# Optimization experiments

Hardware: AMD Instinct MI355X
Metric: run time of the kernel (lower is better)

Reference implementation:

```python
import jax, jax.numpy as jnp
import numpy as np

B, L, H, G, NH, DH, FF = 16, 512, 1024, 2, 16, 64, 4096
DM = H // G          # per-group d_model = 512
LG = L // G          # inner attention seq len = 256
EPS = 1e-6


def _ln(x, g, b):
    m = x.mean(-1, keepdims=True)
    v = ((x - m) ** 2).mean(-1, keepdims=True)
    return (x - m) * jax.lax.rsqrt(v + EPS) * g + b


def setup_inputs() -> dict:
    key = jax.random.key(0)
    ks = jax.random.split(key, 12)
    sd = 0.02
    n = lambda k, sh: jax.random.normal(k, sh, jnp.float32) * sd
    return {
        "y": jax.random.normal(ks[0], (B, L, H), jnp.float32),
        "y_mask": jax.random.randint(ks[1], (B, 1, 1, LG), 0, 2).astype(bool),
        # MHAtt projections (operate on per-group d_model = DM)
        "Wv": n(ks[2], (DM, DM)), "bv": jnp.zeros((DM,), jnp.float32),
        "Wk": n(ks[3], (DM, DM)), "bk": jnp.zeros((DM,), jnp.float32),
        "Wq": n(ks[4], (DM, DM)), "bq": jnp.zeros((DM,), jnp.float32),
        # merge projection (full hidden)
        "Wm": n(ks[5], (H, H)), "bm": jnp.zeros((H,), jnp.float32),
        # GFFN: linear1 H->FF, linear2 grouped FF/G -> H/G
        "W1": n(ks[6], (H, FF)), "b1": jnp.zeros((FF,), jnp.float32),
        "W2": n(ks[7], (FF // G, H // G)), "b2": jnp.zeros((H // G,), jnp.float32),
        # LayerNorms
        "g1": jnp.ones((H,), jnp.float32), "beta1": jnp.zeros((H,), jnp.float32),
        "g2": jnp.ones((H,), jnp.float32), "beta2": jnp.zeros((H,), jnp.float32),
    }


def reference(y, y_mask, Wv, bv, Wk, bk, Wq, bq, Wm, bm, W1, b1, W2, b2,
              g1, beta1, g2, beta2):
    b, l, d = y.shape
    # group reshuffle: split channels into G groups, stack along batch
    yg = jnp.concatenate(jnp.split(y, G, axis=-1), axis=0)        # (b*G, l, DM)
    mask = jnp.tile(y_mask, (G, 1, 1, 1))                          # (b*G, 1, 1, l/G)

    # projections; view uses h*dh = H so inner seq becomes l/G
    q = (yg @ Wq + bq).reshape(b * G, -1, NH, DH).transpose(0, 2, 1, 3)  # (bG, NH, l/G, DH)
    k = (yg @ Wk + bk).reshape(b * G, -1, NH, DH).transpose(0, 2, 1, 3)
    v = (yg @ Wv + bv).reshape(b * G, -1, NH, DH).transpose(0, 2, 1, 3)

    scores = jnp.einsum('bhqd,bhkd->bhqk', q, k) / np.sqrt(DH)
    scores = jnp.where(mask, jnp.float32(-1e9), scores)
    att = jax.nn.softmax(scores, axis=-1)                          # dropout = identity (eval)
    ctx = jnp.einsum('bhqk,bhkd->bhqd', att, v)                    # (bG, NH, l/G, DH)
    ctx = ctx.transpose(0, 2, 1, 3).reshape(b * G, -1, DM)         # (bG, l, DM)

    atted = jnp.concatenate(jnp.split(ctx, G, axis=0), axis=-1)    # (b, l, H)
    atted = atted @ Wm + bm
    y1 = _ln(y + atted, g1, beta1)

    # GFFN
    h1 = jax.nn.relu(y1 @ W1 + b1)                                  # (b, l, FF)
    h2 = jnp.einsum('blgf,fo->blgo', h1.reshape(b, l, G, FF // G), W2) + b2
    ff = h2.reshape(b, l, H)
    return _ln(y1 + ff, g2, beta2)
```

## Files before the change

### kernel.cpp

```cpp
#include <hip/hip_runtime.h>
#include <stdint.h>

typedef unsigned short u16;
using us8   = __attribute__((ext_vector_type(8))) unsigned short;
using us4   = __attribute__((ext_vector_type(4))) unsigned short;
using bf16x8 = __attribute__((ext_vector_type(8))) __bf16;
using f32x4 = __attribute__((ext_vector_type(4))) float;

#define DEV static __device__ __forceinline__

DEV float bf2f(u16 u) { union { uint32_t i; float f; } v; v.i = (uint32_t)u << 16; return v.f; }
DEV u16 f2bf(float f) {
    union { float f; uint32_t i; } v; v.f = f;
    uint32_t u = v.i;
    return (u16)((u + 0x7FFFu + ((u >> 16) & 1u)) >> 16);
}

DEV void async16(const u16* g, u16* ldsbase)
{
    __builtin_amdgcn_global_load_lds((const __attribute__((address_space(1))) void*)g,
                                     (__attribute__((address_space(3))) void*)ldsbase, 16, 0, 0);
}

struct DetectArgs { const void* p[18]; int nw[18]; };

__global__ __launch_bounds__(256) void k_detect_all(DetectArgs a, int* flags)
{
    const int b = blockIdx.x;
    const int t = threadIdx.x;
    __shared__ int cnt[4];
    if (t < 4) cnt[t] = 0;
    __syncthreads();
    if (b == 1) {
        const uint8_t* m = (const uint8_t*)a.p[1];
        int c0 = 0, c1 = 0, c2 = 0, c3 = 0;
        for (int i = t; i < 4096; i += 256) {
            uint8_t v = m[i];
            int mod = i & 3;
            if (v == 0x3F && mod == 1) c0++;
            if (v == 0x3F && mod == 3) c1++;
            if (v == 1 && mod != 0) c2++;
            if (v == 1 && mod == 0) c3++;
        }
        atomicAdd(&cnt[0], c0); atomicAdd(&cnt[1], c1); atomicAdd(&cnt[2], c2); atomicAdd(&cnt[3], c3);
        __syncthreads();
        if (t == 0) {
            int mf;
            if (cnt[0] > 0) mf = 2;
            else if (cnt[1] > 0) mf = 3;
            else if (cnt[2] > 0) mf = 0;
            else if (cnt[3] > 0) mf = 1;
            else mf = 0;
            flags[1] = mf;
        }
    } else {
        const u16* p = (const u16*)a.p[b];
        int nw = a.nw[b];
        int nze = 0, pe = 0, nzo = 0;
        for (int i = t; i < nw; i += 256) {
            u16 w = p[i];
            if (w == 0) continue;
            int e = (w >> 7) & 0xFF;
            bool pl = (e >= 90 && e <= 140);
            if ((i & 1) == 0) { nze++; if (pl) pe++; }
            else nzo++;
        }
        atomicAdd(&cnt[0], nze); atomicAdd(&cnt[1], pe); atomicAdd(&cnt[2], nzo);
        __syncthreads();
        if (t == 0) {
            int f;
            if (cnt[0] > 0)      f = (cnt[1] * 10 >= cnt[0] * 6) ? 2 : 3;
            else if (cnt[2] > 0) f = 3;
            else                 f = 2;
            flags[b] = f;
        }
    }
}

__global__ __launch_bounds__(256) void k_expand_mask(const void* mask, const int* flag, float* mb)
{
    int i = blockIdx.x * 256 + threadIdx.x;
    if (i >= 4096) return;
    int f = *flag;
    bool on;
    if (f == 0)      on = ((const uint8_t*)mask)[i]  != 0;
    else if (f == 1) on = ((const int*)mask)[i]      != 0;
    else if (f == 2) on = ((const u16*)mask)[i]      != 0;
    else             on = ((const uint32_t*)mask)[i] != 0;
    mb[i] = on ? -1e9f : 0.0f;
}

__global__ __launch_bounds__(256) void k_convert_bf(const void* src, u16* dst, int n, const int* flag)
{
    int i = blockIdx.x * 256 + threadIdx.x;
    if (i >= n) return;
    if (*flag == 2) dst[i] = ((const u16*)src)[i];
    else            dst[i] = f2bf(((const float*)src)[i]);
}

struct TransArgs { const void* src[6]; u16* dst[6]; int R[6]; int C[6]; int flagidx[6]; int tstart[7]; };

__global__ __launch_bounds__(256) void k_transpose_all(TransArgs a, const int* flags)
{
    const int tb = blockIdx.x;
    int s = 0;
    while (tb >= a.tstart[s + 1]) s++;
    const int lt = tb - a.tstart[s];
    const int R = a.R[s], C = a.C[s];
    const int tilesX = C >> 5;
    const int ti = lt / tilesX, tj = lt - ti * tilesX;
    const int r0 = ti * 32, c0 = tj * 32;
    const bool isbf = (flags[a.flagidx[s]] == 2);
    const int t = threadIdx.x;
    const int j = t & 31, i0 = t >> 5;
    __shared__ u16 tile[32][33];
#pragma unroll
    for (int p = 0; p < 4; p++) {
        int r = r0 + i0 + p * 8;
        size_t idx = (size_t)r * C + c0 + j;
        u16 v = isbf ? ((const u16*)a.src[s])[idx] : f2bf(((const float*)a.src[s])[idx]);
        tile[i0 + p * 8][j] = v;
    }
    __syncthreads();
    u16* dst = a.dst[s];
#pragma unroll
    for (int p = 0; p < 4; p++) {
        int c = i0 + p * 8;
        dst[(size_t)(c0 + c) * R + r0 + j] = tile[j][c];
    }
}

struct ConvArgs { const void* src[10]; int flagidx[10]; int off[10]; int n[10]; };

__global__ __launch_bounds__(256) void k_convert_params(ConvArgs a, const int* flags, float* par)
{
    int i = blockIdx.x * 256 + threadIdx.x;
    if (i >= 11264) return;
    int s = 0;
    while (s < 9 && i >= a.off[s] + a.n[s]) s++;
    int j = i - a.off[s];
    float v;
    if (flags[a.flagidx[s]] == 2) v = bf2f(((const u16*)a.src[s])[j]);
    else                          v = ((const float*)a.src[s])[j];
    par[i] = v;
}

template<int BM, int BN, int WR, int WC, int TM, int TN>
DEV void gemm_tile(const u16* __restrict__ A, int lda,
                   const u16* __restrict__ Bt, int ldb, int K,
                   u16* As, u16* Bs, f32x4 (&acc)[TM][TN])
{
    const int t = threadIdx.x;
    const int lane = t & 63;
    const int wave = t >> 6;
    const int wr = wave / WC;
    const int wc = wave % WC;
    const int m16 = lane & 15;
    const int quad = lane >> 4;
    const int lr8 = lane >> 3;
    const int lsw = (((lane & 7) ^ lr8) << 3);

#pragma unroll
    for (int i = 0; i < TM; i++)
#pragma unroll
        for (int j = 0; j < TN; j++) {
            acc[i][j][0] = 0.f; acc[i][j][1] = 0.f; acc[i][j][2] = 0.f; acc[i][j][3] = 0.f;
        }

    for (int kb = 0; kb < K; kb += 64) {
#pragma unroll
        for (int i = 0; i < BM / 32; i++) {
            int chunk = wave * (BM / 32) + i;
            int r = chunk * 8 + lr8;
            async16(A + (size_t)r * lda + kb + lsw, As + chunk * 512);
        }
#pragma unroll
        for (int i = 0; i < BN / 32; i++) {
            int chunk = wave * (BN / 32) + i;
            int r = chunk * 8 + lr8;
            async16(Bt + (size_t)r * ldb + kb + lsw, Bs + chunk * 512);
        }
        __syncthreads();
#pragma unroll
        for (int ks = 0; ks < 2; ks++) {
            bf16x8 af[TM], bfr[TN];
#pragma unroll
            for (int i = 0; i < TM; i++) {
                int row = wr * TM * 16 + i * 16 + m16;
                int jq = ks * 4 + quad;
                af[i] = *(const bf16x8*)(As + row * 64 + ((jq ^ (row & 7)) << 3));
            }
#pragma unroll
            for (int j = 0; j < TN; j++) {
                int row = wc * TN * 16 + j * 16 + m16;
                int jq = ks * 4 + quad;
                bfr[j] = *(const bf16x8*)(Bs + row * 64 + ((jq ^ (row & 7)) << 3));
            }
#pragma unroll
            for (int i = 0; i < TM; i++)
#pragma unroll
                for (int j = 0; j < TN; j++)
                    acc[i][j] = __builtin_amdgcn_mfma_f32_16x16x32_bf16(af[i], bfr[j], acc[i][j], 0, 0, 0);
        }
        __syncthreads();
    }
}

template<bool RELU>
__global__ __launch_bounds__(256) void k_gemm_std(const u16* __restrict__ A, int lda,
                                                  const u16* __restrict__ Bt, int ldb,
                                                  const float* __restrict__ bias,
                                                  u16* __restrict__ C, int ldc, int K)
{
    __shared__ __align__(16) u16 As[128 * 64];
    __shared__ __align__(16) u16 Bs[128 * 64];
    const u16* Ab = A + (size_t)blockIdx.y * 128 * lda;
    const u16* Bb = Bt + (size_t)blockIdx.x * 128 * ldb;
    f32x4 acc[4][4];
    gemm_tile<128, 128, 2, 2, 4, 4>(Ab, lda, Bb, ldb, K, As, Bs, acc);

    const int t = threadIdx.x, lane = t & 63, wave = t >> 6;
    const int wr = wave >> 1, wc = wave & 1, m16 = lane & 15, quad = lane >> 4;
    const size_t rowBase = (size_t)blockIdx.y * 128 + wr * 64;
    const int colBase = blockIdx.x * 128 + wc * 64;
#pragma unroll
    for (int tm = 0; tm < 4; tm++)
#pragma unroll
        for (int tn = 0; tn < 4; tn++) {
            int col = colBase + tn * 16 + m16;
            float bv = bias ? bias[col] : 0.f;
#pragma unroll
            for (int r = 0; r < 4; r++) {
                size_t row = rowBase + tm * 16 + quad * 4 + r;
                float v = acc[tm][tn][r] + bv;
                if (RELU) v = fmaxf(v, 0.f);
                C[row * (size_t)ldc + col] = f2bf(v);
            }
        }
}

__global__ __launch_bounds__(256) void k_gemm_qkv(const u16* __restrict__ y_c,
                                                  const u16* __restrict__ WqT,
                                                  const u16* __restrict__ WkT,
                                                  const u16* __restrict__ WvT,
                                                  const float* __restrict__ biases,
                                                  u16* __restrict__ qp, u16* __restrict__ kp, u16* __restrict__ vp)
{
    __shared__ __align__(16) u16 As[128 * 64];
    __shared__ __align__(16) u16 Bs[128 * 64];
    const int z = blockIdx.z;
    const int mat = z % 3, g = z / 3;
    const u16* Bt = (mat == 0) ? WqT : (mat == 1) ? WkT : WvT;
    u16* out = ((mat == 0) ? qp : (mat == 1) ? kp : vp) + (size_t)g * 4194304;
    const float* bias = biases + mat * 512;
    const u16* Ab = y_c + g * 512 + (size_t)blockIdx.y * 128 * 1024;
    const u16* Bb = Bt + (size_t)blockIdx.x * 128 * 512;
    f32x4 acc[4][4];
    gemm_tile<128, 128, 2, 2, 4, 4>(Ab, 1024, Bb, 512, 512, As, Bs, acc);

    const int t = threadIdx.x, lane = t & 63, wave = t >> 6;
    const int wr = wave >> 1, wc = wave & 1, m16 = lane & 15, quad = lane >> 4;
    const size_t rowBase = (size_t)blockIdx.y * 128 + wr * 64;
    const int colBase = blockIdx.x * 128 + wc * 64;
#pragma unroll
    for (int tm = 0; tm < 4; tm++)
#pragma unroll
        for (int tn = 0; tn < 4; tn++) {
            int col = colBase + tn * 16 + m16;
            float bv = bias[col];
#pragma unroll
            for (int r = 0; r < 4; r++) {
                size_t row = rowBase + tm * 16 + quad * 4 + r;
                out[row * 512 + col] = f2bf(acc[tm][tn][r] + bv);
            }
        }
}

__global__ __launch_bounds__(256) void k_attn_scores(const u16* __restrict__ qproj,
                                                     const u16* __restrict__ kproj,
                                                     const float* __restrict__ maskb,
                                                     u16* __restrict__ P)
{
    __shared__ __align__(16) u16 As[64 * 64];
    __shared__ __align__(16) u16 Bs[256 * 64];
    __shared__ float smax[64][5];
    __shared__ float ssum[64][5];
    const int rt = blockIdx.x;
    const int z = blockIdx.y;
    const int bg = z >> 4, h = z & 15, hbit = h >> 3, hlow = h & 7;
    const int b = bg & 15;
    const size_t base = (size_t)bg * 262144 + (size_t)hbit * 512 + (size_t)hlow * 64;
    const u16* A = qproj + base + (size_t)rt * 64 * 1024;
    const u16* B = kproj + base;
    f32x4 acc[4][4];
    gemm_tile<64, 256, 1, 4, 4, 4>(A, 1024, B, 1024, 64, As, Bs, acc);

    const int t = threadIdx.x, lane = t & 63, wc = t >> 6;
    const int m16 = lane & 15, quad = lane >> 4;

    float mb[4];
#pragma unroll
    for (int j = 0; j < 4; j++) mb[j] = maskb[b * 256 + wc * 64 + j * 16 + m16];
#pragma unroll
    for (int i = 0; i < 4; i++)
#pragma unroll
        for (int j = 0; j < 4; j++)
#pragma unroll
            for (int r = 0; r < 4; r++)
                acc[i][j][r] = acc[i][j][r] * 0.125f + mb[j];

#pragma unroll
    for (int i = 0; i < 4; i++)
#pragma unroll
        for (int r = 0; r < 4; r++) {
            float mm = fmaxf(fmaxf(acc[i][0][r], acc[i][1][r]), fmaxf(acc[i][2][r], acc[i][3][r]));
            mm = fmaxf(mm, __shfl_xor(mm, 1));
            mm = fmaxf(mm, __shfl_xor(mm, 2));
            mm = fmaxf(mm, __shfl_xor(mm, 4));
            mm = fmaxf(mm, __shfl_xor(mm, 8));
            if (m16 == 0) smax[i * 16 + quad * 4 + r][wc] = mm;
        }
    __syncthreads();
    float mrow[4][4];
#pragma unroll
    for (int i = 0; i < 4; i++)
#pragma unroll
        for (int r = 0; r < 4; r++) {
            int row = i * 16 + quad * 4 + r;
            mrow[i][r] = fmaxf(fmaxf(smax[row][0], smax[row][1]), fmaxf(smax[row][2], smax[row][3]));
        }
#pragma unroll
    for (int i = 0; i < 4; i++)
#pragma unroll
        for (int r = 0; r < 4; r++) {
            float s = 0.f;
#pragma unroll
            for (int j = 0; j < 4; j++) {
                float e = __expf(acc[i][j][r] - mrow[i][r]);
                acc[i][j][r] = e;
                s += e;
            }
            s += __shfl_xor(s, 1);
            s += __shfl_xor(s, 2);
            s += __shfl_xor(s, 4);
            s += __shfl_xor(s, 8);
            if (m16 == 0) ssum[i * 16 + quad * 4 + r][wc] = s;
        }
    __syncthreads();
    u16* out = P + (size_t)z * 65536 + (size_t)rt * 64 * 256;
#pragma unroll
    for (int i = 0; i < 4; i++)
#pragma unroll
        for (int r = 0; r < 4; r++) {
            int row = i * 16 + quad * 4 + r;
            float inv = 1.0f / (ssum[row][0] + ssum[row][1] + ssum[row][2] + ssum[row][3]);
#pragma unroll
            for (int j = 0; j < 4; j++) {
                int col = wc * 64 + j * 16 + m16;
                out[(size_t)row * 256 + col] = f2bf(acc[i][j][r] * inv);
            }
        }
}

__global__ __launch_bounds__(256) void k_transpose_v(const u16* __restrict__ vproj, u16* __restrict__ vT)
{
    __shared__ __align__(16) u16 tile[64 * 72];
    const int lt = blockIdx.x, hlow = blockIdx.y, bg = blockIdx.z;
    const int t = threadIdx.x;
    {
        int rl = t >> 2, c16 = (t & 3) * 16;
        const u16* src = vproj + (size_t)bg * 262144 + (size_t)(lt * 64 + rl) * 512 + hlow * 64 + c16;
        *(us8*)(tile + rl * 72 + c16)     = *(const us8*)src;
        *(us8*)(tile + rl * 72 + c16 + 8) = *(const us8*)(src + 8);
    }
    __syncthreads();
    const int lanej = t & 31, grp = t >> 5;
#pragma unroll
    for (int hbit = 0; hbit < 2; hbit++) {
        int h = hbit * 8 + hlow;
#pragma unroll
        for (int i = 0; i < 8; i++) {
            int dh = grp + i * 8;
            u16 val = tile[(2 * lanej + hbit) * 72 + dh];
            vT[(((size_t)bg * 16 + h) * 64 + dh) * 256 + lt * 32 + lanej] = val;
        }
    }
}

__global__ __launch_bounds__(256) void k_gemm_ctx(const u16* __restrict__ P,
                                                  const u16* __restrict__ vT,
                                                  u16* __restrict__ attedpre)
{
    __shared__ __align__(16) u16 As[128 * 64];
    __shared__ __align__(16) u16 Bs[64 * 64];
    const int z = blockIdx.y;
    const u16* A = P + (size_t)z * 65536 + (size_t)blockIdx.x * 128 * 256;
    const u16* B = vT + (size_t)z * 16384;
    f32x4 acc[2][4];
    gemm_tile<128, 64, 4, 1, 2, 4>(A, 256, B, 256, 256, As, Bs, acc);

    const int t = threadIdx.x, lane = t & 63, wave = t >> 6;
    const int m16 = lane & 15, quad = lane >> 4;
    const int bg = z >> 4, h = z & 15;
    const int g = bg >> 4, b = bg & 15, hbit = h >> 3, hlow = h & 7;
    const int cBase = g * 512 + hlow * 64;
#pragma unroll
    for (int tm = 0; tm < 2; tm++)
#pragma unroll
        for (int tn = 0; tn < 4; tn++) {
            int dh = tn * 16 + m16;
#pragma unroll
            for (int r = 0; r < 4; r++) {
                int s = blockIdx.x * 128 + wave * 32 + tm * 16 + quad * 4 + r;
                int l = 2 * s + hbit;
                attedpre[((size_t)b * 512 + l) * 1024 + cBase + dh] = f2bf(acc[tm][tn][r]);
            }
        }
}

__global__ __launch_bounds__(256) void k_gemm_ffn2(const u16* __restrict__ h1,
                                                   const u16* __restrict__ W2T,
                                                   const float* __restrict__ b2,
                                                   u16* __restrict__ out)
{
    __shared__ __align__(16) u16 As[128 * 64];
    __shared__ __align__(16) u16 Bs[128 * 64];
    const int xi = blockIdx.x;
    const int g = xi >> 2, xn = xi & 3;
    const u16* Ab = h1 + (size_t)blockIdx.y * 128 * 4096 + g * 2048;
    const u16* Bb = W2T + (size_t)xn * 128 * 2048;
    f32x4 acc[4][4];
    gemm_tile<128, 128, 2, 2, 4, 4>(Ab, 4096, Bb, 2048, 2048, As, Bs, acc);

    const int t = threadIdx.x, lane = t & 63, wave = t >> 6;
    const int wr = wave >> 1, wc = wave & 1, m16 = lane & 15, quad = lane >> 4;
    const size_t rowBase = (size_t)blockIdx.y * 128 + wr * 64;
    const int colg = xn * 128 + wc * 64;
#pragma unroll
    for (int tm = 0; tm < 4; tm++)
#pragma unroll
        for (int tn = 0; tn < 4; tn++) {
            int cg = colg + tn * 16 + m16;
            float bv = b2[cg];
#pragma unroll
            for (int r = 0; r < 4; r++) {
                size_t row = rowBase + tm * 16 + quad * 4 + r;
                out[row * 1024 + g * 512 + cg] = f2bf(acc[tm][tn][r] + bv);
            }
        }
}

template<int FINAL>
__global__ __launch_bounds__(256) void k_ln(const u16* __restrict__ x1, const u16* __restrict__ x2,
                                            const float* __restrict__ gamma, const float* __restrict__ beta,
                                            void* __restrict__ outv, const int* __restrict__ yflag)
{
    const size_t row = blockIdx.x;
    const int t = threadIdx.x;
    us4 a = *(const us4*)(x1 + row * 1024 + t * 4);
    us4 b = *(const us4*)(x2 + row * 1024 + t * 4);
    float v[4]; float s = 0.f, s2 = 0.f;
#pragma unroll
    for (int i = 0; i < 4; i++) { v[i] = bf2f(a[i]) + bf2f(b[i]); s += v[i]; s2 += v[i] * v[i]; }
#pragma unroll
    for (int off = 32; off > 0; off >>= 1) { s += __shfl_xor(s, off); s2 += __shfl_xor(s2, off); }
    __shared__ float red[8];
    const int lane = t & 63, wave = t >> 6;
    if (lane == 0) { red[wave] = s; red[wave + 4] = s2; }
    __syncthreads();
    s = red[0] + red[1] + red[2] + red[3];
    s2 = red[4] + red[5] + red[6] + red[7];
    float mean = s * (1.0f / 1024.0f);
    float var = fmaxf(s2 * (1.0f / 1024.0f) - mean * mean, 0.0f);
    float rs = rsqrtf(var + 1e-6f);
    float o[4];
#pragma unroll
    for (int i = 0; i < 4; i++) {
        int c = t * 4 + i;
        o[i] = (v[i] - mean) * rs * gamma[c] + beta[c];
    }
    bool f32out = FINAL && yflag && (*yflag == 3);
    if (f32out) {
        float* out = (float*)outv;
#pragma unroll
        for (int i = 0; i < 4; i++) out[row * 1024 + t * 4 + i] = o[i];
    } else {
        u16* out = (u16*)outv;
        us4 ov;
#pragma unroll
        for (int i = 0; i < 4; i++) ov[i] = f2bf(o[i]);
        *(us4*)(out + row * 1024 + t * 4) = ov;
    }
}

extern "C" void kernel_launch(void* const* d_in, const int* in_sizes, int n_in,
                              void* d_out, int out_size, void* d_ws, size_t ws_size,
                              hipStream_t stream)
{
    (void)in_sizes; (void)n_in; (void)out_size; (void)ws_size;
    const void* y    = d_in[0];
    const void* mask = d_in[1];
    const void* Wv = d_in[2];  const void* bv = d_in[3];
    const void* Wk = d_in[4];  const void* bk = d_in[5];
    const void* Wq = d_in[6];  const void* bq = d_in[7];
    const void* Wm = d_in[8];  const void* bm = d_in[9];
    const void* W1 = d_in[10]; const void* b1 = d_in[11];
    const void* W2 = d_in[12]; const void* b2 = d_in[13];
    const void* g1 = d_in[14]; const void* be1 = d_in[15];
    const void* g2 = d_in[16]; const void* be2 = d_in[17];

    char* ws = (char*)d_ws;
    size_t off = 0;
    auto alloc = [&](size_t bytes) { void* p = ws + off; off = (off + bytes + 255) & ~(size_t)255; return p; };

    int*   flags = (int*)alloc(32 * 4);
    float* maskb = (float*)alloc(16 * 256 * 4);
    float* par   = (float*)alloc(11264 * 4);
    u16* WqT  = (u16*)alloc((size_t)262144 * 2);
    u16* WkT  = (u16*)alloc((size_t)262144 * 2);
    u16* WvT  = (u16*)alloc((size_t)262144 * 2);
    u16* WmT  = (u16*)alloc((size_t)1048576 * 2);
    u16* W1T  = (u16*)alloc((size_t)4194304 * 2);
    u16* W2T  = (u16*)alloc((size_t)1048576 * 2);
    u16* y_c  = (u16*)alloc((size_t)8388608 * 2);
    u16* slotA = (u16*)alloc((size_t)8388608 * 2);
    u16* slotB = (u16*)alloc((size_t)8388608 * 2);
    u16* slotC = (u16*)alloc((size_t)8388608 * 2);
    u16* slotD = (u16*)alloc((size_t)8388608 * 2);
    u16* Pbig  = (u16*)alloc((size_t)33554432 * 2);

    float* p_bm  = par + 1536;
    float* p_b1  = par + 2560;
    float* p_b2  = par + 6656;
    float* p_g1  = par + 7168;
    float* p_be1 = par + 8192;
    float* p_g2  = par + 9216;
    float* p_be2 = par + 10240;

    DetectArgs da;
    {
        const void* srcs[18] = {y, mask, Wv, bv, Wk, bk, Wq, bq, Wm, bm, W1, b1, W2, b2, g1, be1, g2, be2};
        const int   nele[18] = {8388608, 4096, 262144, 512, 262144, 512, 262144, 512, 1048576, 1024,
                                4194304, 4096, 1048576, 512, 1024, 1024, 1024, 1024};
        for (int i = 0; i < 18; i++) { da.p[i] = srcs[i]; da.nw[i] = nele[i] < 4096 ? nele[i] : 4096; }
    }
    k_detect_all<<<18, 256, 0, stream>>>(da, flags);

    k_expand_mask<<<16, 256, 0, stream>>>(mask, flags + 1, maskb);
    k_convert_bf<<<32768, 256, 0, stream>>>(y, y_c, 8388608, flags + 0);

    TransArgs ta;
    {
        const void* s6[6] = {Wq, Wk, Wv, Wm, W1, W2};
        u16* d6[6] = {WqT, WkT, WvT, WmT, W1T, W2T};
        int R6[6] = {512, 512, 512, 1024, 1024, 2048};
        int C6[6] = {512, 512, 512, 1024, 4096, 512};
        int f6[6] = {6, 4, 2, 8, 10, 12};
        int ts[7] = {0, 256, 512, 768, 1792, 5888, 6912};
        for (int i = 0; i < 6; i++) { ta.src[i] = s6[i]; ta.dst[i] = d6[i]; ta.R[i] = R6[i]; ta.C[i] = C6[i]; ta.flagidx[i] = f6[i]; }
        for (int i = 0; i < 7; i++) ta.tstart[i] = ts[i];
    }
    k_transpose_all<<<6912, 256, 0, stream>>>(ta, flags);

    ConvArgs ca;
    {
        const void* s10[10] = {bq, bk, bv, bm, b1, b2, g1, be1, g2, be2};
        int f10[10] = {7, 5, 3, 9, 11, 13, 14, 15, 16, 17};
        int o10[10] = {0, 512, 1024, 1536, 2560, 6656, 7168, 8192, 9216, 10240};
        int n10[10] = {512, 512, 512, 1024, 4096, 512, 1024, 1024, 1024, 1024};
        for (int i = 0; i < 10; i++) { ca.src[i] = s10[i]; ca.flagidx[i] = f10[i]; ca.off[i] = o10[i]; ca.n[i] = n10[i]; }
    }
    k_convert_params<<<44, 256, 0, stream>>>(ca, flags, par);

    u16* qproj = slotA;
    u16* kproj = slotB;
    u16* vT    = slotC;
    u16* vproj = slotD;

    k_gemm_qkv<<<dim3(4, 64, 6), 256, 0, stream>>>(y_c, WqT, WkT, WvT, par, qproj, kproj, vproj);
    k_transpose_v<<<dim3(8, 8, 32), 256, 0, stream>>>(vproj, vT);

    u16* P = Pbig;
    k_attn_scores<<<dim3(4, 512), 256, 0, stream>>>(qproj, kproj, maskb, P);

    u16* attedpre = slotD;
    k_gemm_ctx<<<dim3(2, 512), 256, 0, stream>>>(P, vT, attedpre);

    u16* mergeout = slotA;
    k_gemm_std<false><<<dim3(8, 64), 256, 0, stream>>>(attedpre, 1024, WmT, 1024, p_bm, mergeout, 1024, 1024);

    u16* y1 = slotB;
    k_ln<0><<<8192, 256, 0, stream>>>(y_c, mergeout, p_g1, p_be1, y1, nullptr);

    u16* h1 = Pbig;
    k_gemm_std<true><<<dim3(32, 64), 256, 0, stream>>>(y1, 1024, W1T, 1024, p_b1, h1, 4096, 1024);

    u16* ffout = slotC;
    k_gemm_ffn2<<<dim3(8, 64), 256, 0, stream>>>(h1, W2T, p_b2, ffout);

    k_ln<1><<<8192, 256, 0, stream>>>(y1, ffout, p_g2, p_be2, d_out, flags + 0);
}
```

Baseline: 475.9 us.

## Use 256x256 double-buffered 8-wave GEMM for the FFN1 projection

Adds a new GEMM kernel with a 256x256 output tile, 512 threads (8 waves), double-buffered LDS staging via async global-to-LDS loads interleaved across four compute quarters, and s_setprio around MFMA bursts. It replaces the 128x128 kernel for the largest GEMM (y1 @ W1 with ReLU). The larger tile raises arithmetic intensity and data reuse, and the staging schedule overlaps loads with MFMA work. In exchange it uses 64KB of LDS per block and more accumulator registers, which limits occupancy, and the grid shrinks to 512 blocks.

Result: slower. 492.2 us (+3.4%).

```diff
diff --git a/kernel.cpp b/kernel.cpp
--- a/kernel.cpp
+++ b/kernel.cpp
@@ -239,6 +239,119 @@
         }
 }
 
+template<bool RELU>
+__global__ __launch_bounds__(512, 2) void k_gemm256(const u16* __restrict__ A, int lda,
+                                                    const u16* __restrict__ Bt, int ldb,
+                                                    const float* __restrict__ bias,
+                                                    u16* __restrict__ C, int ldc, int K)
+{
+    __shared__ __align__(16) u16 As[2][256 * 64];
+    __shared__ __align__(16) u16 Bs[2][256 * 64];
+    const int t = threadIdx.x;
+    const int lane = t & 63, wave = t >> 6;
+    const int wr = wave >> 2, wc = wave & 3;
+    const int m16 = lane & 15, quad = lane >> 4;
+    const int lr8 = lane >> 3;
+    const int lsw = (((lane & 7) ^ lr8) << 3);
+
+    const u16* __restrict__ Ab = A + (size_t)blockIdx.y * 256 * lda;
+    const u16* __restrict__ Bb = Bt + (size_t)blockIdx.x * 256 * ldb;
+
+    f32x4 acc[8][4];
+#pragma unroll
+    for (int i = 0; i < 8; i++)
+#pragma unroll
+        for (int j = 0; j < 4; j++) {
+            acc[i][j][0] = 0.f; acc[i][j][1] = 0.f; acc[i][j][2] = 0.f; acc[i][j][3] = 0.f;
+        }
+
+    const int NT = K >> 6;
+
+    auto stage_half = [&](int kb, int c, int h) {
+        const u16* src = (h < 2) ? Ab : Bb;
+        const int ld   = (h < 2) ? lda : ldb;
+        u16* dst = (h < 2) ? &As[c][0] : &Bs[c][0];
+#pragma unroll
+        for (int r = 0; r < 2; r++) {
+            int chunk = (h & 1) * 16 + r * 8 + wave;
+            int row = chunk * 8 + lr8;
+            async16(src + (size_t)row * ld + kb + lsw, dst + chunk * 512);
+        }
+    };
+
+#pragma unroll
+    for (int h = 0; h < 4; h++) stage_half(0, 0, h);
+    if (NT > 1) {
+        stage_half(64, 1, 0);
+        asm volatile("s_waitcnt vmcnt(2)" ::: "memory");
+    } else {
+        asm volatile("s_waitcnt vmcnt(0)" ::: "memory");
+    }
+    asm volatile("s_barrier" ::: "memory");
+
+    for (int kt = 0; kt < NT; ++kt) {
+        const int c = kt & 1, n = c ^ 1;
+        const int kb1 = (kt + 1) << 6;
+        const bool st1 = (kt + 1 < NT);
+#pragma unroll
+        for (int q = 0; q < 4; q++) {
+            if (st1 && q < 3) stage_half(kb1, n, q + 1);
+            const int mq = q >> 1, nq = q & 1;
+            bf16x8 af[2][4], bfr[2][2];
+#pragma unroll
+            for (int ks = 0; ks < 2; ks++) {
+                int jq = ks * 4 + quad;
+#pragma unroll
+                for (int i = 0; i < 4; i++) {
+                    int row = wr * 128 + (mq * 4 + i) * 16 + m16;
+                    af[ks][i] = *(const bf16x8*)(&As[c][row * 64 + ((jq ^ (row & 7)) << 3)]);
+                }
+#pragma unroll
+                for (int j = 0; j < 2; j++) {
+                    int row = wc * 64 + (nq * 2 + j) * 16 + m16;
+                    bfr[ks][j] = *(const bf16x8*)(&Bs[c][row * 64 + ((jq ^ (row & 7)) << 3)]);
+                }
+            }
+            __builtin_amdgcn_s_setprio(1);
+#pragma unroll
+            for (int ks = 0; ks < 2; ks++)
+#pragma unroll
+                for (int i = 0; i < 4; i++)
+#pragma unroll
+                    for (int j = 0; j < 2; j++)
+                        acc[mq * 4 + i][nq * 2 + j] =
+                            __builtin_amdgcn_mfma_f32_16x16x32_bf16(af[ks][i], bfr[ks][j],
+                                                                    acc[mq * 4 + i][nq * 2 + j], 0, 0, 0);
+            __builtin_amdgcn_s_setprio(0);
+            asm volatile("s_barrier" ::: "memory");
+        }
+        if (kt + 2 < NT) {
+            stage_half((kt + 2) << 6, c, 0);
+            asm volatile("s_waitcnt vmcnt(2)" ::: "memory");
+        } else {
+            asm volatile("s_waitcnt vmcnt(0)" ::: "memory");
+        }
+        asm volatile("s_barrier" ::: "memory");
+    }
+
+    const size_t rowBase = (size_t)blockIdx.y * 256 + wr * 128;
+    const int colBase = blockIdx.x * 256 + wc * 64;
+#pragma unroll
+    for (int f = 0; f < 8; f++)
+#pragma unroll
+        for (int tn = 0; tn < 4; tn++) {
+            int col = colBase + tn * 16 + m16;
+            float bv = bias ? bias[col] : 0.f;
+#pragma unroll
+            for (int r = 0; r < 4; r++) {
+                size_t row = rowBase + f * 16 + quad * 4 + r;
+                float v = acc[f][tn][r] + bv;
+                if (RELU) v = fmaxf(v, 0.f);
+                C[row * (size_t)ldc + col] = f2bf(v);
+            }
+        }
+}
+
 __global__ __launch_bounds__(256) void k_gemm_qkv(const u16* __restrict__ y_c,
                                                   const u16* __restrict__ WqT,
                                                   const u16* __restrict__ WkT,
@@ -593,7 +706,7 @@
     k_ln<0><<<8192, 256, 0, stream>>>(y_c, mergeout, p_g1, p_be1, y1, nullptr);
 
     u16* h1 = Pbig;
-    k_gemm_std<true><<<dim3(32, 64), 256, 0, stream>>>(y1, 1024, W1T, 1024, p_b1, h1, 4096, 1024);
+    k_gemm256<true><<<dim3(16, 32), 512, 0, stream>>>(y1, 1024, W1T, 1024, p_b1, h1, 4096, 1024);
 
     u16* ffout = slotC;
     k_gemm_ffn2<<<dim3(8, 64), 256, 0, stream>>>(h1, W2T, p_b2, ffout);
```

## Fuse attention scores, softmax and context GEMM into one kernel

Applied to the files above, without the earlier changes.

Replaces the separate scores+softmax kernel and context GEMM with one fused kernel per (batch-group, head). K and V^T are staged into LDS with XOR-swizzled async loads, and scores are kept in registers. Each wave stages normalized probabilities through a per-wave LDS buffer before the P·V MFMA. This removes the write and re-read of the full bf16 probability matrix in global memory and one launch. The cost is heavy register pressure from the 2x16 score tiles with 512-thread blocks, and only 512 blocks in the grid.

Result: faster. 423.8 us (-11.0%).

```diff
diff --git a/kernel.cpp b/kernel.cpp
--- a/kernel.cpp
+++ b/kernel.cpp
@@ -276,92 +276,6 @@
         }
 }
 
-__global__ __launch_bounds__(256) void k_attn_scores(const u16* __restrict__ qproj,
-                                                     const u16* __restrict__ kproj,
-                                                     const float* __restrict__ maskb,
-                                                     u16* __restrict__ P)
-{
-    __shared__ __align__(16) u16 As[64 * 64];
-    __shared__ __align__(16) u16 Bs[256 * 64];
-    __shared__ float smax[64][5];
-    __shared__ float ssum[64][5];
-    const int rt = blockIdx.x;
-    const int z = blockIdx.y;
-    const int bg = z >> 4, h = z & 15, hbit = h >> 3, hlow = h & 7;
-    const int b = bg & 15;
-    const size_t base = (size_t)bg * 262144 + (size_t)hbit * 512 + (size_t)hlow * 64;
-    const u16* A = qproj + base + (size_t)rt * 64 * 1024;
-    const u16* B = kproj + base;
-    f32x4 acc[4][4];
-    gemm_tile<64, 256, 1, 4, 4, 4>(A, 1024, B, 1024, 64, As, Bs, acc);
-
-    const int t = threadIdx.x, lane = t & 63, wc = t >> 6;
-    const int m16 = lane & 15, quad = lane >> 4;
-
-    float mb[4];
-#pragma unroll
-    for (int j = 0; j < 4; j++) mb[j] = maskb[b * 256 + wc * 64 + j * 16 + m16];
-#pragma unroll
-    for (int i = 0; i < 4; i++)
-#pragma unroll
-        for (int j = 0; j < 4; j++)
-#pragma unroll
-            for (int r = 0; r < 4; r++)
-                acc[i][j][r] = acc[i][j][r] * 0.125f + mb[j];
-
-#pragma unroll
-    for (int i = 0; i < 4; i++)
-#pragma unroll
-        for (int r = 0; r < 4; r++) {
-            float mm = fmaxf(fmaxf(acc[i][0][r], acc[i][1][r]), fmaxf(acc[i][2][r], acc[i][3][r]));
-            mm = fmaxf(mm, __shfl_xor(mm, 1));
-            mm = fmaxf(mm, __shfl_xor(mm, 2));
-            mm = fmaxf(mm, __shfl_xor(mm, 4));
-            mm = fmaxf(mm, __shfl_xor(mm, 8));
-            if (m16 == 0) smax[i * 16 + quad * 4 + r][wc] = mm;
-        }
-    __syncthreads();
-    float mrow[4][4];
-#pragma unroll
-    for (int i = 0; i < 4; i++)
-#pragma unroll
-        for (int r = 0; r < 4; r++) {
-            int row = i * 16 + quad * 4 + r;
-            mrow[i][r] = fmaxf(fmaxf(smax[row][0], smax[row][1]), fmaxf(smax[row][2], smax[row][3]));
-        }
-#pragma unroll
-    for (int i = 0; i < 4; i++)
-#pragma unroll
-        for (int r = 0; r < 4; r++) {
-            float s = 0.f;
-#pragma unroll
-            for (int j = 0; j < 4; j++) {
-                float e = __expf(acc[i][j][r] - mrow[i][r]);
-                acc[i][j][r] = e;
-                s += e;
-            }
-            s += __shfl_xor(s, 1);
-            s += __shfl_xor(s, 2);
-            s += __shfl_xor(s, 4);
-            s += __shfl_xor(s, 8);
-            if (m16 == 0) ssum[i * 16 + quad * 4 + r][wc] = s;
-        }
-    __syncthreads();
-    u16* out = P + (size_t)z * 65536 + (size_t)rt * 64 * 256;
-#pragma unroll
-    for (int i = 0; i < 4; i++)
-#pragma unroll
-        for (int r = 0; r < 4; r++) {
-            int row = i * 16 + quad * 4 + r;
-            float inv = 1.0f / (ssum[row][0] + ssum[row][1] + ssum[row][2] + ssum[row][3]);
-#pragma unroll
-            for (int j = 0; j < 4; j++) {
-                int col = wc * 64 + j * 16 + m16;
-                out[(size_t)row * 256 + col] = f2bf(acc[i][j][r] * inv);
-            }
-        }
-}
-
 __global__ __launch_bounds__(256) void k_transpose_v(const u16* __restrict__ vproj, u16* __restrict__ vT)
 {
     __shared__ __align__(16) u16 tile[64 * 72];
@@ -387,33 +301,161 @@
     }
 }
 
-__global__ __launch_bounds__(256) void k_gemm_ctx(const u16* __restrict__ P,
-                                                  const u16* __restrict__ vT,
-                                                  u16* __restrict__ attedpre)
-{
-    __shared__ __align__(16) u16 As[128 * 64];
-    __shared__ __align__(16) u16 Bs[64 * 64];
-    const int z = blockIdx.y;
-    const u16* A = P + (size_t)z * 65536 + (size_t)blockIdx.x * 128 * 256;
-    const u16* B = vT + (size_t)z * 16384;
-    f32x4 acc[2][4];
-    gemm_tile<128, 64, 4, 1, 2, 4>(A, 256, B, 256, 256, As, Bs, acc);
-
+__global__ __launch_bounds__(512, 2) void k_attn_fused(const u16* __restrict__ qproj,
+                                                       const u16* __restrict__ kproj,
+                                                       const u16* __restrict__ vT,
+                                                       const float* __restrict__ maskb,
+                                                       u16* __restrict__ attedpre)
+{
+    __shared__ __align__(16) u16 Ks[256 * 64];
+    __shared__ __align__(16) u16 Vs[64 * 256];
+    __shared__ __align__(16) u16 Ps[8 * 2 * 2048];
+
+    const int z = blockIdx.x;
+    const int bg = z >> 4, h = z & 15, hbit = h >> 3, hlow = h & 7;
+    const int b = bg & 15, g = bg >> 4;
     const int t = threadIdx.x, lane = t & 63, wave = t >> 6;
     const int m16 = lane & 15, quad = lane >> 4;
-    const int bg = z >> 4, h = z & 15;
-    const int g = bg >> 4, b = bg & 15, hbit = h >> 3, hlow = h & 7;
+    const int lr8 = lane >> 3;
+    const int lsw = (((lane & 7) ^ lr8) << 3);
+
+    const size_t base = (size_t)bg * 262144 + (size_t)hbit * 512 + (size_t)hlow * 64;
+    const u16* Qb = qproj + base;
+    const u16* Kb = kproj + base;
+
+#pragma unroll
+    for (int i = 0; i < 4; i++) {
+        int chunk = wave * 4 + i;
+        int row = chunk * 8 + lr8;
+        async16(Kb + (size_t)row * 1024 + lsw, Ks + chunk * 512);
+    }
+    const u16* Vb = vT + (size_t)z * 16384;
+#pragma unroll
+    for (int i = 0; i < 4; i++) {
+        int chunk = wave * 4 + i;
+        int d = chunk * 2 + (lane >> 5);
+        int jl = lane & 31;
+        int jsrc = (jl & 24) | ((jl & 7) ^ (d & 7));
+        async16(Vb + (size_t)d * 256 + jsrc * 8, Vs + chunk * 512);
+    }
+
+    bf16x8 qf[2][2];
+#pragma unroll
+    for (int mt = 0; mt < 2; mt++)
+#pragma unroll
+        for (int ks = 0; ks < 2; ks++) {
+            int qrow = wave * 32 + mt * 16 + m16;
+            qf[mt][ks] = *(const bf16x8*)(Qb + (size_t)qrow * 1024 + ks * 32 + quad * 8);
+        }
+    float mb[16];
+#pragma unroll
+    for (int nt = 0; nt < 16; nt++) mb[nt] = maskb[b * 256 + nt * 16 + m16];
+
+    __syncthreads();
+
+    f32x4 s[2][16];
+#pragma unroll
+    for (int mt = 0; mt < 2; mt++)
+#pragma unroll
+        for (int nt = 0; nt < 16; nt++) { s[mt][nt][0] = 0.f; s[mt][nt][1] = 0.f; s[mt][nt][2] = 0.f; s[mt][nt][3] = 0.f; }
+#pragma unroll
+    for (int ks = 0; ks < 2; ks++) {
+        int jq = ks * 4 + quad;
+#pragma unroll
+        for (int nt = 0; nt < 16; nt++) {
+            int row = nt * 16 + m16;
+            bf16x8 kf = *(const bf16x8*)(Ks + row * 64 + ((jq ^ (row & 7)) << 3));
+#pragma unroll
+            for (int mt = 0; mt < 2; mt++)
+                s[mt][nt] = __builtin_amdgcn_mfma_f32_16x16x32_bf16(qf[mt][ks], kf, s[mt][nt], 0, 0, 0);
+        }
+    }
+
+    float rinv[2][4];
+#pragma unroll
+    for (int mt = 0; mt < 2; mt++)
+#pragma unroll
+        for (int r = 0; r < 4; r++) {
+            float mm = -3.0e38f;
+#pragma unroll
+            for (int nt = 0; nt < 16; nt++) {
+                float v = s[mt][nt][r] * 0.125f + mb[nt];
+                s[mt][nt][r] = v;
+                mm = fmaxf(mm, v);
+            }
+            mm = fmaxf(mm, __shfl_xor(mm, 1));
+            mm = fmaxf(mm, __shfl_xor(mm, 2));
+            mm = fmaxf(mm, __shfl_xor(mm, 4));
+            mm = fmaxf(mm, __shfl_xor(mm, 8));
+            float ss = 0.f;
+#pragma unroll
+            for (int nt = 0; nt < 16; nt++) {
+                float e = __expf(s[mt][nt][r] - mm);
+                s[mt][nt][r] = e;
+                ss += e;
+            }
+            ss += __shfl_xor(ss, 1);
+            ss += __shfl_xor(ss, 2);
+            ss += __shfl_xor(ss, 4);
+            ss += __shfl_xor(ss, 8);
+            rinv[mt][r] = 1.0f / ss;
+        }
+
+    f32x4 ctx[2][4];
+#pragma unroll
+    for (int mt = 0; mt < 2; mt++)
+#pragma unroll
+        for (int dt = 0; dt < 4; dt++) { ctx[mt][dt][0] = 0.f; ctx[mt][dt][1] = 0.f; ctx[mt][dt][2] = 0.f; ctx[mt][dt][3] = 0.f; }
+
+#pragma unroll
+    for (int kc = 0; kc < 4; kc++) {
+        u16* Pb = Ps + wave * 4096 + (kc & 1) * 2048;
+#pragma unroll
+        for (int mt = 0; mt < 2; mt++)
+#pragma unroll
+            for (int nl = 0; nl < 4; nl++) {
+                int nt = kc * 4 + nl;
+#pragma unroll
+                for (int r = 0; r < 4; r++) {
+                    int row = mt * 16 + quad * 4 + r;
+                    int col = nl * 16 + m16;
+                    int j = col >> 3, e = col & 7;
+                    Pb[row * 64 + (((j ^ (row & 7)) << 3) | e)] = f2bf(s[mt][nt][r] * rinv[mt][r]);
+                }
+            }
+#pragma unroll
+        for (int ks = 0; ks < 2; ks++) {
+            int jq = ks * 4 + quad;
+            bf16x8 pf[2];
+#pragma unroll
+            for (int mt = 0; mt < 2; mt++) {
+                int row = mt * 16 + m16;
+                pf[mt] = *(const bf16x8*)(Pb + row * 64 + ((jq ^ (row & 7)) << 3));
+            }
+#pragma unroll
+            for (int dt = 0; dt < 4; dt++) {
+                int d = dt * 16 + m16;
+                int j = kc * 8 + ks * 4 + quad;
+                int slot = (j & 24) | ((j & 7) ^ (d & 7));
+                bf16x8 vf = *(const bf16x8*)(Vs + d * 256 + slot * 8);
+#pragma unroll
+                for (int mt = 0; mt < 2; mt++)
+                    ctx[mt][dt] = __builtin_amdgcn_mfma_f32_16x16x32_bf16(pf[mt], vf, ctx[mt][dt], 0, 0, 0);
+            }
+        }
+    }
+
     const int cBase = g * 512 + hlow * 64;
 #pragma unroll
-    for (int tm = 0; tm < 2; tm++)
-#pragma unroll
-        for (int tn = 0; tn < 4; tn++) {
-            int dh = tn * 16 + m16;
+    for (int mt = 0; mt < 2; mt++)
+#pragma unroll
+        for (int dt = 0; dt < 4; dt++) {
+            int dh = dt * 16 + m16;
 #pragma unroll
             for (int r = 0; r < 4; r++) {
-                int s = blockIdx.x * 128 + wave * 32 + tm * 16 + quad * 4 + r;
-                int l = 2 * s + hbit;
-                attedpre[((size_t)b * 512 + l) * 1024 + cBase + dh] = f2bf(acc[tm][tn][r]);
+                int sI = wave * 32 + mt * 16 + quad * 4 + r;
+                int l = 2 * sI + hbit;
+                attedpre[((size_t)b * 512 + l) * 1024 + cBase + dh] = f2bf(ctx[mt][dt][r]);
             }
         }
 }
@@ -580,11 +622,8 @@
     k_gemm_qkv<<<dim3(4, 64, 6), 256, 0, stream>>>(y_c, WqT, WkT, WvT, par, qproj, kproj, vproj);
     k_transpose_v<<<dim3(8, 8, 32), 256, 0, stream>>>(vproj, vT);
 
-    u16* P = Pbig;
-    k_attn_scores<<<dim3(4, 512), 256, 0, stream>>>(qproj, kproj, maskb, P);
-
     u16* attedpre = slotD;
-    k_gemm_ctx<<<dim3(2, 512), 256, 0, stream>>>(P, vT, attedpre);
+    k_attn_fused<<<512, 512, 0, stream>>>(qproj, kproj, vT, maskb, attedpre);
 
     u16* mergeout = slotA;
     k_gemm_std<false><<<dim3(8, 64), 256, 0, stream>>>(attedpre, 1024, WmT, 1024, p_bm, mergeout, 1024, 1024);
```
